# Kernel optimization log

Hardware: AMD Instinct MI355X
Metric: run time of the kernel (lower is better)

The kernel has to match this reference:

```python
import jax, jax.numpy as jnp
import numpy as np

HEADS = 16
D_MODEL = 1024
D_K = D_MODEL // HEADS


def setup_inputs() -> dict:
    key = jax.random.key(0)
    ks = jax.random.split(key, 8)
    B, S = 4, 2048
    scale = 1.0 / np.sqrt(D_MODEL)
    return {
        "queries": jax.random.normal(ks[0], (B, S, D_MODEL), dtype=jnp.float32),
        "keys": jax.random.normal(ks[1], (B, S, D_MODEL), dtype=jnp.float32),
        "values": jax.random.normal(ks[2], (B, S, D_MODEL), dtype=jnp.float32),
        # Per-head projection weights, stacked over heads: [H, d_model, d_k]
        "Wq": jax.random.normal(ks[3], (HEADS, D_MODEL, D_K), dtype=jnp.float32) * scale,
        "Wk": jax.random.normal(ks[4], (HEADS, D_MODEL, D_K), dtype=jnp.float32) * scale,
        "Wv": jax.random.normal(ks[5], (HEADS, D_MODEL, D_K), dtype=jnp.float32) * scale,
        "Wout": jax.random.normal(ks[6], (D_MODEL, D_MODEL), dtype=jnp.float32) * scale,
        "bout": jax.random.normal(ks[7], (D_MODEL,), dtype=jnp.float32) * 0.01,
    }


def reference(queries, keys, values, Wq, Wk, Wv, Wout, bout):
    # Per-head linear projections (torch Linear: x @ W.T, here W stored as [H, d_model, d_k])
    q = jnp.einsum("bsd,hdk->bhsk", queries, Wq)   # [B,H,S,d_k]
    k = jnp.einsum("btd,hdk->bhtk", keys, Wk)      # [B,H,T,d_k]
    v = jnp.einsum("btd,hdv->bhtv", values, Wv)    # [B,H,T,d_v]
    scores = jnp.einsum("bhsk,bhtk->bhst", q, k) / jnp.sqrt(jnp.float32(D_K))
    probs = jax.nn.softmax(scores, axis=-1)        # [B,H,S,T]
    wv = jnp.einsum("bhst,bhtv->bhsv", probs, v)   # [B,H,S,d_v]
    # concat heads along last dim: [B,S,H*d_v] == [B,S,d_model]
    B, H, S, Dv = wv.shape
    concat = jnp.transpose(wv, (0, 2, 1, 3)).reshape(B, S, H * Dv)
    return concat @ Wout.T + bout
```

## Files before the change

### kernel.cpp

```cpp
#include <hip/hip_runtime.h>
#include <hip/hip_bf16.h>
#include <stdint.h>

#define DM 1024
#define SZ ((size_t)8192*1024)
#define WSZ ((size_t)1024*1024)

typedef float  f32x2  __attribute__((ext_vector_type(2)));
typedef float  f32x4  __attribute__((ext_vector_type(4)));
typedef float  f32x16 __attribute__((ext_vector_type(16)));
typedef __bf16 bf16x8 __attribute__((ext_vector_type(8)));
typedef __bf16 bf16x2 __attribute__((ext_vector_type(2)));
typedef short  s16x8  __attribute__((ext_vector_type(8)));
typedef unsigned int u32;
typedef unsigned int u32x4 __attribute__((ext_vector_type(4)));

typedef const __attribute__((address_space(1))) void* gas_ptr;
typedef __attribute__((address_space(3))) void* las_ptr;

static __device__ __forceinline__ f32x4 mfma16(s16x8 a, s16x8 b, f32x4 c){
  return __builtin_amdgcn_mfma_f32_16x16x32_bf16(
      __builtin_bit_cast(bf16x8, a), __builtin_bit_cast(bf16x8, b), c, 0, 0, 0);
}
static __device__ __forceinline__ f32x16 mfma32(s16x8 a, s16x8 b, f32x16 c){
  return __builtin_amdgcn_mfma_f32_32x32x16_bf16(
      __builtin_bit_cast(bf16x8, a), __builtin_bit_cast(bf16x8, b), c, 0, 0, 0);
}

static __device__ __forceinline__ u32 pack2(float a, float b){
  bf16x2 v = { (__bf16)a, (__bf16)b };
  return __builtin_bit_cast(u32, v);
}
static __device__ __forceinline__ short f2bf(float f){
  __bf16 v = (__bf16)f;
  return __builtin_bit_cast(short, v);
}

static __device__ __forceinline__ void gload_lds16(void* l, const void* g){
  __builtin_amdgcn_global_load_lds((gas_ptr)g, (las_ptr)l, 16, 0, 0);
}

#define QSCALE 0.1803368801111444f


__global__ void convert_misc(const float* __restrict__ q, const float* __restrict__ k,
                             const float* __restrict__ v, const float* __restrict__ wo,
                             short* __restrict__ ws){
  size_t c = (size_t)blockIdx.x*blockDim.x + threadIdx.x;
  const size_t n8_in = 3*(SZ/8);
  const float* src; short* dst;
  if (c < n8_in){
    int s = (int)(c >> 20);
    size_t off = c*8 - ((size_t)s << 23);
    src = (s==0 ? q : (s==1 ? k : v)) + off;
    dst = ws + c*8;
  } else {
    size_t off = (c - n8_in)*8;
    src = wo + off;
    dst = ws + 6*SZ + 3*WSZ + off;
  }
  float4 a = *(const float4*)src;
  float4 b = *(const float4*)(src + 4);
  uint4 o;
  o.x = pack2(a.x, a.y); o.y = pack2(a.z, a.w);
  o.z = pack2(b.x, b.y); o.w = pack2(b.z, b.w);
  *(uint4*)dst = o;
}

__global__ void convert_wqkv(const float* __restrict__ wq, const float* __restrict__ wk,
                             const float* __restrict__ wv, short* __restrict__ ws){
  __shared__ float tile[64][65];
  int bid = blockIdx.x;
  int sel = bid >> 8;
  int h   = (bid >> 4) & 15;
  int dt  = bid & 15;
  const float* W = sel==0 ? wq : (sel==1 ? wk : wv);
  float sc = sel==0 ? QSCALE : 1.0f;
  short* Bt = ws + 6*SZ + (size_t)sel*WSZ;
  int tid = threadIdx.x;
  int r = tid >> 4, c4 = (tid & 15)*4;
  int d0 = dt*64;
  #pragma unroll
  for (int i=0;i<4;i++){
    int d = r + i*16;
    float4 vv = *(const float4*)&W[(size_t)h*65536 + (size_t)(d0+d)*64 + c4];
    tile[d][c4+0]=vv.x*sc; tile[d][c4+1]=vv.y*sc; tile[d][c4+2]=vv.z*sc; tile[d][c4+3]=vv.w*sc;
  }
  __syncthreads();
  #pragma unroll
  for (int i=0;i<4;i++){
    int kk = r + i*16;
    unsigned int lo = pack2(tile[c4+0][kk], tile[c4+1][kk]);
    unsigned int hi = pack2(tile[c4+2][kk], tile[c4+3][kk]);
    *(uint2*)&Bt[(size_t)(h*64+kk)*1024 + d0 + c4] = make_uint2(lo, hi);
  }
}


static __device__ __forceinline__ void gemm_core_bf16(
    const short* __restrict__ A, const short* __restrict__ Bt,
    int bm, int bn, short* As, short* Bs, f32x4 acc[4][4])
{
  int tid = threadIdx.x;
  int w = tid>>6, lane = tid&63;
  int wm = w>>1, wn = w&1;
  int col = lane&15, kg = lane>>4;
  int rs = w*16 + (lane>>2);
  int ch = lane&3;
  int chs = ch ^ (rs & 3);

  auto stage = [&](int buf, int kt){
    #pragma unroll
    for (int it=0; it<2; ++it){
      int r = rs + it*64;
      gload_lds16(As + buf*4096 + r*32 + ch*8,
                  A + (size_t)(bm*128 + r)*1024 + kt*32 + chs*8);
    }
    #pragma unroll
    for (int it=0; it<2; ++it){
      int r = rs + it*64;
      gload_lds16(Bs + buf*4096 + r*32 + ch*8,
                  Bt + (size_t)(bn*128 + r)*1024 + kt*32 + chs*8);
    }
  };

  const f32x4 fzero = {0.f,0.f,0.f,0.f};
  #pragma unroll
  for (int mf=0; mf<4; ++mf)
    #pragma unroll
    for (int nf=0; nf<4; ++nf)
      acc[mf][nf] = fzero;

  int fbase = col*32 + ((kg ^ (col&3))<<3);

  stage(0, 0);
  int buf = 0;
  for (int kt=0; kt<32; ++kt){
    __syncthreads();
    if (kt < 31) stage(buf^1, kt+1);
    s16x8 af[4], bfr[4];
    #pragma unroll
    for (int mf=0; mf<4; ++mf)
      af[mf] = *(const s16x8*)(As + buf*4096 + (wm*64 + mf*16)*32 + fbase);
    #pragma unroll
    for (int nf=0; nf<4; ++nf)
      bfr[nf] = *(const s16x8*)(Bs + buf*4096 + (wn*64 + nf*16)*32 + fbase);
    #pragma unroll
    for (int mf=0; mf<4; ++mf)
      #pragma unroll
      for (int nf=0; nf<4; ++nf)
        acc[mf][nf] = mfma16(af[mf], bfr[nf], acc[mf][nf]);
    buf ^= 1;
  }
}

__global__ __launch_bounds__(256,2) void gemm_qkv(short* __restrict__ ws){
  __shared__ __align__(16) short As[2*4096];
  __shared__ __align__(16) short Bs[2*4096];
  int bid = blockIdx.x;
  bid = (bid & 7)*192 + (bid >> 3);
  int bm = bid / 24, bnq = bid % 24;
  int sel = bnq >> 3, bn = bnq & 7;
  const short* A  = ws + (size_t)sel*SZ;
  const short* Bt = ws + 6*SZ + (size_t)sel*WSZ;
  f32x4 acc[4][4];
  gemm_core_bf16(A, Bt, bm, bn, As, Bs, acc);

  int tid = threadIdx.x, w = tid>>6, lane = tid&63;
  int wm=w>>1, wn=w&1, col=lane&15, kg=lane>>4;
  if (sel == 0){
    short* O = ws + 3*SZ;
    #pragma unroll
    for (int mf=0; mf<4; ++mf){
      int gr0 = bm*128 + wm*64 + mf*16 + kg*4;
      #pragma unroll
      for (int nf=0; nf<4; ++nf){
        int gc = bn*128 + wn*64 + nf*16 + col;
        #pragma unroll
        for (int r=0; r<4; ++r)
          O[(size_t)(gr0+r)*1024 + gc] = f2bf(acc[mf][nf][r]);
      }
    }
  } else if (sel == 1){
    short* Kt = ws + 4*SZ;
    #pragma unroll
    for (int mf=0; mf<4; ++mf){
      int gr0 = bm*128 + wm*64 + mf*16 + kg*4;
      int b = gr0 >> 11, s0 = gr0 & 2047;
      int ts = s0 >> 5, t0 = s0 & 31;
      #pragma unroll
      for (int nf=0; nf<4; ++nf){
        int gc = bn*128 + wn*64 + nf*16 + col;
        int h = gc >> 6, d = gc & 63;
        size_t base = ((size_t)((b*16+h)*64 + ts))*2048 + (size_t)((d>>3)*32)*8 + (d&7);
        #pragma unroll
        for (int r=0; r<4; ++r)
          Kt[base + (size_t)(t0+r)*8] = f2bf(acc[mf][nf][r]);
      }
    }
  } else {
    short* Vt = ws + 5*SZ;
    #pragma unroll
    for (int mf=0; mf<4; ++mf){
      int gr0 = bm*128 + wm*64 + mf*16 + kg*4;
      int b = gr0 >> 11, s0 = gr0 & 2047;
      int ts = s0 >> 5, c2 = (s0 >> 3) & 3, j0 = s0 & 7;
      #pragma unroll
      for (int nf=0; nf<4; ++nf){
        int gc = bn*128 + wn*64 + nf*16 + col;
        int h = gc >> 6, dv = gc & 63;
        unsigned int lo = pack2(acc[mf][nf][0], acc[mf][nf][1]);
        unsigned int hi = pack2(acc[mf][nf][2], acc[mf][nf][3]);
        size_t addr = ((size_t)((b*16+h)*64 + ts))*2048 + (size_t)(c2*64 + dv)*8 + j0;
        *(uint2*)&Vt[addr] = make_uint2(lo, hi);
      }
    }
  }
}

__global__ __launch_bounds__(256,2) void gemm_out(const short* __restrict__ cc,
                                                  const short* __restrict__ BtO,
                                                  const float* __restrict__ bias,
                                                  float* __restrict__ out){
  __shared__ __align__(16) short As[2*4096];
  __shared__ __align__(16) short Bs[2*4096];
  int bid = blockIdx.x;
  bid = (bid & 7)*64 + (bid >> 3);
  int bm = bid >> 3, bn = bid & 7;
  f32x4 acc[4][4];
  gemm_core_bf16(cc, BtO, bm, bn, As, Bs, acc);

  int tid = threadIdx.x, w=tid>>6, lane=tid&63;
  int wm=w>>1, wn=w&1, col=lane&15, kg=lane>>4;
  #pragma unroll
  for (int nf=0; nf<4; ++nf){
    int gc = bn*128 + wn*64 + nf*16 + col;
    float bb = bias[gc];
    #pragma unroll
    for (int mf=0; mf<4; ++mf){
      int gr0 = bm*128 + wm*64 + mf*16 + kg*4;
      #pragma unroll
      for (int r=0; r<4; ++r)
        out[(size_t)(gr0+r)*1024 + gc] = acc[mf][nf][r] + bb;
    }
  }
}

__global__ __launch_bounds__(256,2) void attn(const short* __restrict__ qp,
                                              const short* __restrict__ kpT,
                                              const short* __restrict__ vTt,
                                              short* __restrict__ cc){
  __shared__ __align__(16) short Ks[2][4096];
  __shared__ __align__(16) short Vs[2][4096];
  int bid = blockIdx.x;
  bid = (bid & 7)*128 + (bid >> 3);
  int qb = bid & 15, h = (bid>>4) & 15, b = bid >> 8;
  int bh = b*16 + h;
  int tid = threadIdx.x, w = tid>>6, lane = tid&63;
  int ql = lane & 31, hi = lane >> 5;
  int qbase = qb*128 + w*32;

  const short* qg = qp + ((size_t)(b*2048 + qbase + ql))*1024 + h*64;
  s16x8 qf[4];
  #pragma unroll
  for (int ks=0; ks<4; ++ks)
    qf[ks] = *(const s16x8*)(qg + ks*16 + hi*8);

  const short* ktb = kpT + ((size_t)(bh*64))*2048;
  const short* vtb = vTt + ((size_t)(bh*64))*2048;

  int koff = hi*512 + ql*16;
  int voff = hi*1024 + ql*16;

  int jj = (w & 1) * 2048;
  const short* sgb = ((w < 2) ? ktb : vtb) + jj + lane*8;
  short* ldb = ((w < 2) ? &Ks[0][0] : &Vs[0][0]) + jj + lane*8;
  auto stage = [&](int buf, int ti2){
    const short* src = sgb + (size_t)ti2*4096;
    short* dst = ldb + buf*4096;
    gload_lds16(dst,        src);
    gload_lds16(dst + 512,  src + 512);
    gload_lds16(dst + 1024, src + 1024);
    gload_lds16(dst + 1536, src + 1536);
  };

  const f32x16 z16 = {0.f,0.f,0.f,0.f,0.f,0.f,0.f,0.f,
                      0.f,0.f,0.f,0.f,0.f,0.f,0.f,0.f};
  f32x16 o0 = z16, o1 = z16;
  f32x2 l2 = {0.f, 0.f};

  auto packP = [&](f32x16& s, s16x8* pb){
    u32 a0 = pack2(s[0], s[1]),  b0 = pack2(s[2], s[3]);
    u32 c0 = pack2(s[4], s[5]),  d0 = pack2(s[6], s[7]);
    asm("v_permlane32_swap_b32 %0, %1" : "+v"(a0), "+v"(c0));
    asm("v_permlane32_swap_b32 %0, %1" : "+v"(b0), "+v"(d0));
    u32x4 t0v = {a0, b0, c0, d0};
    pb[0] = __builtin_bit_cast(s16x8, t0v);
    u32 a1 = pack2(s[8], s[9]),   b1 = pack2(s[10], s[11]);
    u32 c1 = pack2(s[12], s[13]), d1 = pack2(s[14], s[15]);
    asm("v_permlane32_swap_b32 %0, %1" : "+v"(a1), "+v"(c1));
    asm("v_permlane32_swap_b32 %0, %1" : "+v"(b1), "+v"(d1));
    u32x4 t1v = {a1, b1, c1, d1};
    pb[1] = __builtin_bit_cast(s16x8, t1v);
  };

  auto body = [&](int buf){
    const char* kt = (const char*)Ks + buf*8192;
    const char* vt = (const char*)Vs + buf*8192;
    f32x16 s0 = z16, s1 = z16;
    __builtin_amdgcn_s_setprio(1);
    #pragma unroll
    for (int ks=0; ks<4; ++ks){
      s16x8 kf0 = *(const s16x8*)(kt + koff + ks*1024);
      s16x8 kf1 = *(const s16x8*)(kt + 4096 + koff + ks*1024);
      s0 = mfma32(kf0, qf[ks], s0);
      s1 = mfma32(kf1, qf[ks], s1);
    }
    __builtin_amdgcn_s_setprio(0);

    f32x2 la = {0.f,0.f}, lb = {0.f,0.f};
    #pragma unroll
    for (int i=0;i<16;i+=4){
      s0[i]   = __builtin_amdgcn_exp2f(s0[i]);
      s0[i+1] = __builtin_amdgcn_exp2f(s0[i+1]);
      s0[i+2] = __builtin_amdgcn_exp2f(s0[i+2]);
      s0[i+3] = __builtin_amdgcn_exp2f(s0[i+3]);
      f32x2 pa = {s0[i], s0[i+1]}, pbv = {s0[i+2], s0[i+3]};
      la += pa; lb += pbv;
    }
    #pragma unroll
    for (int i=0;i<16;i+=4){
      s1[i]   = __builtin_amdgcn_exp2f(s1[i]);
      s1[i+1] = __builtin_amdgcn_exp2f(s1[i+1]);
      s1[i+2] = __builtin_amdgcn_exp2f(s1[i+2]);
      s1[i+3] = __builtin_amdgcn_exp2f(s1[i+3]);
      f32x2 pa = {s1[i], s1[i+1]}, pbv = {s1[i+2], s1[i+3]};
      la += pa; lb += pbv;
    }
    l2 += la + lb;

    s16x8 pb[4];
    packP(s0, pb);
    packP(s1, pb + 2);

    __builtin_amdgcn_s_setprio(1);
    #pragma unroll
    for (int ks2=0; ks2<4; ++ks2){
      const char* vb2 = vt + (ks2>>1)*4096 + (ks2&1)*2048 + voff;
      s16x8 vf0 = *(const s16x8*)(vb2);
      s16x8 vf1 = *(const s16x8*)(vb2 + 512);
      o0 = mfma32(vf0, pb[ks2], o0);
      o1 = mfma32(vf1, pb[ks2], o1);
    }
    __builtin_amdgcn_s_setprio(0);
  };

  stage(0, 0);
  for (int ti = 0; ti < 32; ++ti){
    __syncthreads();
    if (ti < 31) stage((ti&1)^1, ti+1);
    body(ti&1);
  }

  float l = l2[0] + l2[1];
  l += __shfl_xor(l, 32);
  float rcl = 1.0f / l;
  short* og = cc + ((size_t)(b*2048 + qbase + ql))*1024 + h*64;
  #pragma unroll
  for (int s=0; s<4; ++s){
    int dv0 = s*8 + hi*4;
    uint2 w0, w1;
    w0.x = pack2(o0[s*4+0]*rcl, o0[s*4+1]*rcl);
    w0.y = pack2(o0[s*4+2]*rcl, o0[s*4+3]*rcl);
    *(uint2*)&og[dv0] = w0;
    w1.x = pack2(o1[s*4+0]*rcl, o1[s*4+1]*rcl);
    w1.y = pack2(o1[s*4+2]*rcl, o1[s*4+3]*rcl);
    *(uint2*)&og[32 + dv0] = w1;
  }
}


extern "C" void kernel_launch(void* const* d_in, const int* in_sizes, int n_in,
                              void* d_out, int out_size, void* d_ws, size_t ws_size,
                              hipStream_t stream){
  const float* q  = (const float*)d_in[0];
  const float* k  = (const float*)d_in[1];
  const float* v  = (const float*)d_in[2];
  const float* wq = (const float*)d_in[3];
  const float* wk = (const float*)d_in[4];
  const float* wv = (const float*)d_in[5];
  const float* wo = (const float*)d_in[6];
  const float* bo = (const float*)d_in[7];
  short* ws = (short*)d_ws;
  float* out = (float*)d_out;

  size_t needed = (6*SZ + 4*WSZ)*sizeof(short);
  if (ws_size < needed) return;

  convert_misc<<<12800, 256, 0, stream>>>(q, k, v, wo, ws);
  convert_wqkv<<<768, 256, 0, stream>>>(wq, wk, wv, ws);
  gemm_qkv<<<1536, 256, 0, stream>>>(ws);
  attn<<<1024, 256, 0, stream>>>(ws + 3*SZ, ws + 4*SZ, ws + 5*SZ, ws);
  gemm_out<<<512, 256, 0, stream>>>(ws, ws + 6*SZ + 3*WSZ, bo, out);
}
```

Before: 203.3 us.

## Load K/V fragments directly from global into registers, doubling queries per wave

The attention kernel stops staging K and V tiles through double-buffered LDS with block-wide barriers. Each wave now loads its K and V MFMA fragments straight from global memory into registers, prefetching the next K tile. Each wave handles 64 query rows instead of 32 so every loaded fragment feeds twice as many MFMAs, and the grid is halved to 512 blocks. This removes the LDS traffic and __syncthreads, but each wave now loads K/V itself with no sharing inside the block, relies on cache for reuse, and leaves fewer blocks to fill the GPU.

```diff
diff --git a/kernel.cpp b/kernel.cpp
--- a/kernel.cpp
+++ b/kernel.cpp
@@ -250,44 +250,29 @@
                                               const short* __restrict__ kpT,
                                               const short* __restrict__ vTt,
                                               short* __restrict__ cc){
-  __shared__ __align__(16) short Ks[2][4096];
-  __shared__ __align__(16) short Vs[2][4096];
   int bid = blockIdx.x;
-  bid = (bid & 7)*128 + (bid >> 3);
-  int qb = bid & 15, h = (bid>>4) & 15, b = bid >> 8;
+  bid = (bid & 7)*64 + (bid >> 3);
+  int qb = bid & 7, h = (bid>>3) & 15, b = bid >> 7;
   int bh = b*16 + h;
   int tid = threadIdx.x, w = tid>>6, lane = tid&63;
   int ql = lane & 31, hi = lane >> 5;
-  int qbase = qb*128 + w*32;
+  int qbase = qb*256 + w*64;
 
   const short* qg = qp + ((size_t)(b*2048 + qbase + ql))*1024 + h*64;
-  s16x8 qf[4];
-  #pragma unroll
-  for (int ks=0; ks<4; ++ks)
-    qf[ks] = *(const s16x8*)(qg + ks*16 + hi*8);
-
-  const short* ktb = kpT + ((size_t)(bh*64))*2048;
-  const short* vtb = vTt + ((size_t)(bh*64))*2048;
-
-  int koff = hi*512 + ql*16;
-  int voff = hi*1024 + ql*16;
-
-  int jj = (w & 1) * 2048;
-  const short* sgb = ((w < 2) ? ktb : vtb) + jj + lane*8;
-  short* ldb = ((w < 2) ? &Ks[0][0] : &Vs[0][0]) + jj + lane*8;
-  auto stage = [&](int buf, int ti2){
-    const short* src = sgb + (size_t)ti2*4096;
-    short* dst = ldb + buf*4096;
-    gload_lds16(dst,        src);
-    gload_lds16(dst + 512,  src + 512);
-    gload_lds16(dst + 1024, src + 1024);
-    gload_lds16(dst + 1536, src + 1536);
-  };
+  s16x8 qf[2][4];
+  #pragma unroll
+  for (int qt=0; qt<2; ++qt)
+    #pragma unroll
+    for (int ks=0; ks<4; ++ks)
+      qf[qt][ks] = *(const s16x8*)(qg + qt*32*1024 + ks*16 + hi*8);
+
+  const short* kfb = kpT + (size_t)(bh*64)*2048 + hi*256 + ql*8;
+  const short* vfb = vTt + (size_t)(bh*64)*2048 + hi*512 + ql*8;
 
   const f32x16 z16 = {0.f,0.f,0.f,0.f,0.f,0.f,0.f,0.f,
                       0.f,0.f,0.f,0.f,0.f,0.f,0.f,0.f};
-  f32x16 o0 = z16, o1 = z16;
-  f32x2 l2 = {0.f, 0.f};
+  f32x16 o[2][2] = {{z16, z16}, {z16, z16}};
+  float l0 = 0.f, l1 = 0.f;
 
   auto packP = [&](f32x16& s, s16x8* pb){
     u32 a0 = pack2(s[0], s[1]),  b0 = pack2(s[2], s[3]);
@@ -304,19 +289,33 @@
     pb[1] = __builtin_bit_cast(s16x8, t1v);
   };
 
-  auto body = [&](int buf){
-    const char* kt = (const char*)Ks + buf*8192;
-    const char* vt = (const char*)Vs + buf*8192;
+  s16x8 kf[4];
+  #pragma unroll
+  for (int ks=0; ks<4; ++ks)
+    kf[ks] = *(const s16x8*)(kfb + ks*512);
+
+  for (int ts = 0; ts < 64; ++ts){
+    const short* vsrc = vfb + (size_t)ts*2048;
+    s16x8 vf0 = *(const s16x8*)(vsrc);
+    s16x8 vf1 = *(const s16x8*)(vsrc + 256);
+    s16x8 vf2 = *(const s16x8*)(vsrc + 1024);
+    s16x8 vf3 = *(const s16x8*)(vsrc + 1280);
+
     f32x16 s0 = z16, s1 = z16;
     __builtin_amdgcn_s_setprio(1);
     #pragma unroll
     for (int ks=0; ks<4; ++ks){
-      s16x8 kf0 = *(const s16x8*)(kt + koff + ks*1024);
-      s16x8 kf1 = *(const s16x8*)(kt + 4096 + koff + ks*1024);
-      s0 = mfma32(kf0, qf[ks], s0);
-      s1 = mfma32(kf1, qf[ks], s1);
+      s0 = mfma32(kf[ks], qf[0][ks], s0);
+      s1 = mfma32(kf[ks], qf[1][ks], s1);
     }
     __builtin_amdgcn_s_setprio(0);
+
+    if (ts < 63){
+      const short* ksrc = kfb + (size_t)(ts+1)*2048;
+      #pragma unroll
+      for (int ks=0; ks<4; ++ks)
+        kf[ks] = *(const s16x8*)(ksrc + ks*512);
+    }
 
     f32x2 la = {0.f,0.f}, lb = {0.f,0.f};
     #pragma unroll
@@ -328,6 +327,8 @@
       f32x2 pa = {s0[i], s0[i+1]}, pbv = {s0[i+2], s0[i+3]};
       la += pa; lb += pbv;
     }
+    l0 += (la[0]+la[1]) + (lb[0]+lb[1]);
+    f32x2 lc = {0.f,0.f}, ld = {0.f,0.f};
     #pragma unroll
     for (int i=0;i<16;i+=4){
       s1[i]   = __builtin_amdgcn_exp2f(s1[i]);
@@ -335,47 +336,44 @@
       s1[i+2] = __builtin_amdgcn_exp2f(s1[i+2]);
       s1[i+3] = __builtin_amdgcn_exp2f(s1[i+3]);
       f32x2 pa = {s1[i], s1[i+1]}, pbv = {s1[i+2], s1[i+3]};
-      la += pa; lb += pbv;
-    }
-    l2 += la + lb;
-
-    s16x8 pb[4];
-    packP(s0, pb);
-    packP(s1, pb + 2);
+      lc += pa; ld += pbv;
+    }
+    l1 += (lc[0]+lc[1]) + (ld[0]+ld[1]);
+
+    s16x8 pb0[2], pb1[2];
+    packP(s0, pb0);
+    packP(s1, pb1);
 
     __builtin_amdgcn_s_setprio(1);
-    #pragma unroll
-    for (int ks2=0; ks2<4; ++ks2){
-      const char* vb2 = vt + (ks2>>1)*4096 + (ks2&1)*2048 + voff;
-      s16x8 vf0 = *(const s16x8*)(vb2);
-      s16x8 vf1 = *(const s16x8*)(vb2 + 512);
-      o0 = mfma32(vf0, pb[ks2], o0);
-      o1 = mfma32(vf1, pb[ks2], o1);
-    }
+    o[0][0] = mfma32(vf0, pb0[0], o[0][0]);
+    o[1][0] = mfma32(vf0, pb1[0], o[1][0]);
+    o[0][1] = mfma32(vf1, pb0[0], o[0][1]);
+    o[1][1] = mfma32(vf1, pb1[0], o[1][1]);
+    o[0][0] = mfma32(vf2, pb0[1], o[0][0]);
+    o[1][0] = mfma32(vf2, pb1[1], o[1][0]);
+    o[0][1] = mfma32(vf3, pb0[1], o[0][1]);
+    o[1][1] = mfma32(vf3, pb1[1], o[1][1]);
     __builtin_amdgcn_s_setprio(0);
-  };
-
-  stage(0, 0);
-  for (int ti = 0; ti < 32; ++ti){
-    __syncthreads();
-    if (ti < 31) stage((ti&1)^1, ti+1);
-    body(ti&1);
-  }
-
-  float l = l2[0] + l2[1];
-  l += __shfl_xor(l, 32);
-  float rcl = 1.0f / l;
-  short* og = cc + ((size_t)(b*2048 + qbase + ql))*1024 + h*64;
-  #pragma unroll
-  for (int s=0; s<4; ++s){
-    int dv0 = s*8 + hi*4;
-    uint2 w0, w1;
-    w0.x = pack2(o0[s*4+0]*rcl, o0[s*4+1]*rcl);
-    w0.y = pack2(o0[s*4+2]*rcl, o0[s*4+3]*rcl);
-    *(uint2*)&og[dv0] = w0;
-    w1.x = pack2(o1[s*4+0]*rcl, o1[s*4+1]*rcl);
-    w1.y = pack2(o1[s*4+2]*rcl, o1[s*4+3]*rcl);
-    *(uint2*)&og[32 + dv0] = w1;
+  }
+
+  l0 += __shfl_xor(l0, 32);
+  l1 += __shfl_xor(l1, 32);
+  float rc0 = 1.0f / l0, rc1 = 1.0f / l1;
+  #pragma unroll
+  for (int qt=0; qt<2; ++qt){
+    float rcl = qt ? rc1 : rc0;
+    short* og = cc + ((size_t)(b*2048 + qbase + qt*32 + ql))*1024 + h*64;
+    #pragma unroll
+    for (int dvt=0; dvt<2; ++dvt){
+      #pragma unroll
+      for (int s=0; s<4; ++s){
+        int dv0 = dvt*32 + s*8 + hi*4;
+        uint2 wd;
+        wd.x = pack2(o[qt][dvt][s*4+0]*rcl, o[qt][dvt][s*4+1]*rcl);
+        wd.y = pack2(o[qt][dvt][s*4+2]*rcl, o[qt][dvt][s*4+3]*rcl);
+        *(uint2*)&og[dv0] = wd;
+      }
+    }
   }
 }
 
@@ -400,6 +398,6 @@
   convert_misc<<<12800, 256, 0, stream>>>(q, k, v, wo, ws);
   convert_wqkv<<<768, 256, 0, stream>>>(wq, wk, wv, ws);
   gemm_qkv<<<1536, 256, 0, stream>>>(ws);
-  attn<<<1024, 256, 0, stream>>>(ws + 3*SZ, ws + 4*SZ, ws + 5*SZ, ws);
+  attn<<<512, 256, 0, stream>>>(ws + 3*SZ, ws + 4*SZ, ws + 5*SZ, ws);
   gemm_out<<<512, 256, 0, stream>>>(ws, ws + 6*SZ + 3*WSZ, bo, out);
 }
```

New measurement: 198.3 us. 1.03x faster.

## Load attention K/V fragments straight from global and widen conversion per thread

Applied to the files above, without the earlier changes.

The attention kernel no longer stages K and V tiles through double-buffered LDS behind barriers. Each wave now reads its MFMA fragments directly from global memory, 32 keys per step with K prefetched one step ahead, and launch bounds rise to 4 blocks per CU to hide the latency through occupancy. Separately, the fp32-to-bf16 conversion kernel handles 16 elements per thread with half the grid. The trade is that K/V reuse across the four waves of a block now relies on cache instead of LDS, with more global load instructions in exchange for no barriers.

```diff
diff --git a/kernel.cpp b/kernel.cpp
--- a/kernel.cpp
+++ b/kernel.cpp
@@ -47,24 +47,29 @@
                              const float* __restrict__ v, const float* __restrict__ wo,
                              short* __restrict__ ws){
   size_t c = (size_t)blockIdx.x*blockDim.x + threadIdx.x;
-  const size_t n8_in = 3*(SZ/8);
+  const size_t n16_in = 3*(SZ/16);
   const float* src; short* dst;
-  if (c < n8_in){
-    int s = (int)(c >> 20);
-    size_t off = c*8 - ((size_t)s << 23);
+  if (c < n16_in){
+    int s = (int)(c >> 19);
+    size_t off = c*16 - ((size_t)s << 23);
     src = (s==0 ? q : (s==1 ? k : v)) + off;
-    dst = ws + c*8;
+    dst = ws + c*16;
   } else {
-    size_t off = (c - n8_in)*8;
+    size_t off = (c - n16_in)*16;
     src = wo + off;
     dst = ws + 6*SZ + 3*WSZ + off;
   }
   float4 a = *(const float4*)src;
   float4 b = *(const float4*)(src + 4);
-  uint4 o;
-  o.x = pack2(a.x, a.y); o.y = pack2(a.z, a.w);
-  o.z = pack2(b.x, b.y); o.w = pack2(b.z, b.w);
-  *(uint4*)dst = o;
+  float4 e = *(const float4*)(src + 8);
+  float4 f = *(const float4*)(src + 12);
+  uint4 o0, o1;
+  o0.x = pack2(a.x, a.y); o0.y = pack2(a.z, a.w);
+  o0.z = pack2(b.x, b.y); o0.w = pack2(b.z, b.w);
+  o1.x = pack2(e.x, e.y); o1.y = pack2(e.z, e.w);
+  o1.z = pack2(f.x, f.y); o1.w = pack2(f.z, f.w);
+  *(uint4*)dst = o0;
+  *(uint4*)(dst + 8) = o1;
 }
 
 __global__ void convert_wqkv(const float* __restrict__ wq, const float* __restrict__ wk,
@@ -246,12 +251,10 @@
   }
 }
 
-__global__ __launch_bounds__(256,2) void attn(const short* __restrict__ qp,
+__global__ __launch_bounds__(256,4) void attn(const short* __restrict__ qp,
                                               const short* __restrict__ kpT,
                                               const short* __restrict__ vTt,
                                               short* __restrict__ cc){
-  __shared__ __align__(16) short Ks[2][4096];
-  __shared__ __align__(16) short Vs[2][4096];
   int bid = blockIdx.x;
   bid = (bid & 7)*128 + (bid >> 3);
   int qb = bid & 15, h = (bid>>4) & 15, b = bid >> 8;
@@ -266,28 +269,13 @@
   for (int ks=0; ks<4; ++ks)
     qf[ks] = *(const s16x8*)(qg + ks*16 + hi*8);
 
-  const short* ktb = kpT + ((size_t)(bh*64))*2048;
-  const short* vtb = vTt + ((size_t)(bh*64))*2048;
-
-  int koff = hi*512 + ql*16;
-  int voff = hi*1024 + ql*16;
-
-  int jj = (w & 1) * 2048;
-  const short* sgb = ((w < 2) ? ktb : vtb) + jj + lane*8;
-  short* ldb = ((w < 2) ? &Ks[0][0] : &Vs[0][0]) + jj + lane*8;
-  auto stage = [&](int buf, int ti2){
-    const short* src = sgb + (size_t)ti2*4096;
-    short* dst = ldb + buf*4096;
-    gload_lds16(dst,        src);
-    gload_lds16(dst + 512,  src + 512);
-    gload_lds16(dst + 1024, src + 1024);
-    gload_lds16(dst + 1536, src + 1536);
-  };
+  const short* kfb = kpT + (size_t)(bh*64)*2048 + hi*256 + ql*8;
+  const short* vfb = vTt + (size_t)(bh*64)*2048 + hi*512 + ql*8;
 
   const f32x16 z16 = {0.f,0.f,0.f,0.f,0.f,0.f,0.f,0.f,
                       0.f,0.f,0.f,0.f,0.f,0.f,0.f,0.f};
   f32x16 o0 = z16, o1 = z16;
-  f32x2 l2 = {0.f, 0.f};
+  float l = 0.f;
 
   auto packP = [&](f32x16& s, s16x8* pb){
     u32 a0 = pack2(s[0], s[1]),  b0 = pack2(s[2], s[3]);
@@ -304,19 +292,31 @@
     pb[1] = __builtin_bit_cast(s16x8, t1v);
   };
 
-  auto body = [&](int buf){
-    const char* kt = (const char*)Ks + buf*8192;
-    const char* vt = (const char*)Vs + buf*8192;
-    f32x16 s0 = z16, s1 = z16;
+  s16x8 kf[4];
+  #pragma unroll
+  for (int ks=0; ks<4; ++ks)
+    kf[ks] = *(const s16x8*)(kfb + ks*512);
+
+  for (int ts = 0; ts < 64; ++ts){
+    const short* vsrc = vfb + (size_t)ts*2048;
+    s16x8 vf0 = *(const s16x8*)(vsrc);
+    s16x8 vf1 = *(const s16x8*)(vsrc + 256);
+    s16x8 vf2 = *(const s16x8*)(vsrc + 1024);
+    s16x8 vf3 = *(const s16x8*)(vsrc + 1280);
+
+    f32x16 s0 = z16;
     __builtin_amdgcn_s_setprio(1);
     #pragma unroll
-    for (int ks=0; ks<4; ++ks){
-      s16x8 kf0 = *(const s16x8*)(kt + koff + ks*1024);
-      s16x8 kf1 = *(const s16x8*)(kt + 4096 + koff + ks*1024);
-      s0 = mfma32(kf0, qf[ks], s0);
-      s1 = mfma32(kf1, qf[ks], s1);
-    }
+    for (int ks=0; ks<4; ++ks)
+      s0 = mfma32(kf[ks], qf[ks], s0);
     __builtin_amdgcn_s_setprio(0);
+
+    if (ts < 63){
+      const short* ksrc = kfb + (size_t)(ts+1)*2048;
+      #pragma unroll
+      for (int ks=0; ks<4; ++ks)
+        kf[ks] = *(const s16x8*)(ksrc + ks*512);
+    }
 
     f32x2 la = {0.f,0.f}, lb = {0.f,0.f};
     #pragma unroll
@@ -328,41 +328,20 @@
       f32x2 pa = {s0[i], s0[i+1]}, pbv = {s0[i+2], s0[i+3]};
       la += pa; lb += pbv;
     }
-    #pragma unroll
-    for (int i=0;i<16;i+=4){
-      s1[i]   = __builtin_amdgcn_exp2f(s1[i]);
-      s1[i+1] = __builtin_amdgcn_exp2f(s1[i+1]);
-      s1[i+2] = __builtin_amdgcn_exp2f(s1[i+2]);
-      s1[i+3] = __builtin_amdgcn_exp2f(s1[i+3]);
-      f32x2 pa = {s1[i], s1[i+1]}, pbv = {s1[i+2], s1[i+3]};
-      la += pa; lb += pbv;
-    }
-    l2 += la + lb;
-
-    s16x8 pb[4];
+    la += lb;
+    l += la[0] + la[1];
+
+    s16x8 pb[2];
     packP(s0, pb);
-    packP(s1, pb + 2);
 
     __builtin_amdgcn_s_setprio(1);
-    #pragma unroll
-    for (int ks2=0; ks2<4; ++ks2){
-      const char* vb2 = vt + (ks2>>1)*4096 + (ks2&1)*2048 + voff;
-      s16x8 vf0 = *(const s16x8*)(vb2);
-      s16x8 vf1 = *(const s16x8*)(vb2 + 512);
-      o0 = mfma32(vf0, pb[ks2], o0);
-      o1 = mfma32(vf1, pb[ks2], o1);
-    }
+    o0 = mfma32(vf0, pb[0], o0);
+    o1 = mfma32(vf1, pb[0], o1);
+    o0 = mfma32(vf2, pb[1], o0);
+    o1 = mfma32(vf3, pb[1], o1);
     __builtin_amdgcn_s_setprio(0);
-  };
-
-  stage(0, 0);
-  for (int ti = 0; ti < 32; ++ti){
-    __syncthreads();
-    if (ti < 31) stage((ti&1)^1, ti+1);
-    body(ti&1);
-  }
-
-  float l = l2[0] + l2[1];
+  }
+
   l += __shfl_xor(l, 32);
   float rcl = 1.0f / l;
   short* og = cc + ((size_t)(b*2048 + qbase + ql))*1024 + h*64;
@@ -397,7 +376,7 @@
   size_t needed = (6*SZ + 4*WSZ)*sizeof(short);
   if (ws_size < needed) return;
 
-  convert_misc<<<12800, 256, 0, stream>>>(q, k, v, wo, ws);
+  convert_misc<<<6400, 256, 0, stream>>>(q, k, v, wo, ws);
   convert_wqkv<<<768, 256, 0, stream>>>(wq, wk, wv, ws);
   gemm_qkv<<<1536, 256, 0, stream>>>(ws);
   attn<<<1024, 256, 0, stream>>>(ws + 3*SZ, ws + 4*SZ, ws + 5*SZ, ws);
```

After: 207.4 us. +2.0%, slower.
